# Kernel optimization log

Hardware: AMD Instinct MI355X
Metric: run time of the kernel (lower is better)

Reference implementation:

```python
import jax, jax.numpy as jnp
import numpy as np

B, L, D = 1, 512, 1280


def setup_inputs() -> dict:
    key = jax.random.key(0)
    k1, k2, k3 = jax.random.split(key, 3)
    prev_result = jax.random.normal(k1, (B, L, D), dtype=jnp.float32)
    # nn.Linear(2*D, 2): store weight as [2D, 2] so forward is x @ W + b
    W = jax.random.normal(k2, (2 * D, 2), dtype=jnp.float32) * (1.0 / np.sqrt(2 * D))
    b = jax.random.normal(k3, (2,), dtype=jnp.float32) * 0.01
    return {"prev_result": prev_result, "W": W, "b": b}


def reference(prev_result, W, b):
    # Dropout is identity at inference. The torch code builds
    # pairwise = cat(x_i * x_j, x_i - x_j) of shape [B,L,L,2D] then applies
    # Linear(2D, 2). We fuse: split W into the prod half Wp and diff half Wd.
    Wp, Wd = W[:D], W[D:]                                   # each [D, 2]
    # (x_i * x_j) @ Wp  -- bilinear contraction, no [B,L,L,2D] intermediate
    prod_term = jnp.einsum('bid,bjd,dk->bijk', prev_result, prev_result, Wp)
    # (x_i - x_j) @ Wd = (x @ Wd)_i - (x @ Wd)_j
    d_proj = prev_result @ Wd                                # [B, L, 2]
    diff_term = d_proj[:, :, None, :] - d_proj[:, None, :, :]
    prediction = prod_term + diff_term + b                   # [B, L, L, 2]
    prediction = (prediction + prediction.transpose(0, 2, 1, 3)) / 2
    return prediction[:, 1:-1, 1:-1]                         # [B, L-2, L-2, 2]
```

## Files before the change

kernel.cpp:

```cpp
#include <hip/hip_runtime.h>

#define D_DIM 1280
#define ODIM  510
#define NSTEP (D_DIM / 32)

typedef __attribute__((ext_vector_type(8))) short bf16x8;
typedef __attribute__((ext_vector_type(4))) float f32x4;

__device__ __forceinline__ unsigned pkbf(float a, float b) {
  unsigned ua = __float_as_uint(a), ub = __float_as_uint(b);
  return ((ua + 0x8000u) >> 16) | ((ub + 0x8000u) & 0xffff0000u);
}

__global__ __launch_bounds__(256, 1) void pcmd_prep(
    const float* __restrict__ X,
    const float* __restrict__ W,
    unsigned short* __restrict__ Xbf,
    unsigned short* __restrict__ A0,
    unsigned short* __restrict__ A1)
{
  int t = (int)blockIdx.x * 256 + (int)threadIdx.x;
  int r = t / 160;
  int c = t - r * 160;
  const float* px = X + (size_t)r * D_DIM + c * 8;
  float4 x0 = *(const float4*)px;
  float4 x1 = *(const float4*)(px + 4);
  const float* pw = W + (size_t)c * 16;
  float4 w0 = *(const float4*)(pw +  0);
  float4 w1 = *(const float4*)(pw +  4);
  float4 w2 = *(const float4*)(pw +  8);
  float4 w3 = *(const float4*)(pw + 12);
  size_t o = (size_t)r * D_DIM + c * 8;
  uint4 vx, v0, v1;
  vx.x = pkbf(x0.x, x0.y);            vx.y = pkbf(x0.z, x0.w);
  vx.z = pkbf(x1.x, x1.y);            vx.w = pkbf(x1.z, x1.w);
  v0.x = pkbf(x0.x*w0.x, x0.y*w0.z);  v0.y = pkbf(x0.z*w1.x, x0.w*w1.z);
  v0.z = pkbf(x1.x*w2.x, x1.y*w2.z);  v0.w = pkbf(x1.z*w3.x, x1.w*w3.z);
  v1.x = pkbf(x0.x*w0.y, x0.y*w0.w);  v1.y = pkbf(x0.z*w1.y, x0.w*w1.w);
  v1.z = pkbf(x1.x*w2.y, x1.y*w2.w);  v1.w = pkbf(x1.z*w3.y, x1.w*w3.w);
  *(uint4*)(Xbf + o) = vx;
  *(uint4*)(A0  + o) = v0;
  *(uint4*)(A1  + o) = v1;
}

__global__ __launch_bounds__(256, 1) void pcmd_gemm(
    const unsigned short* __restrict__ Xbf,
    const unsigned short* __restrict__ A0,
    const unsigned short* __restrict__ A1,
    const float* __restrict__ b,
    float* __restrict__ out)
{
  const int tid  = threadIdx.x;
  const int lane = tid & 63;
  const int wv   = tid >> 6;
  const int wi   = wv >> 1;
  const int wj   = wv & 1;
  const int m    = lane & 15;
  const int quad = lane >> 4;

  const int i_base = 1 + (int)blockIdx.y * 32 + wi * 16;
  const int j_base = 1 + (int)blockIdx.x * 32 + wj * 16;
  int gi = i_base + m; if (gi > 511) gi = 511;
  int gj = j_base + m; if (gj > 511) gj = 511;

  const unsigned short* pa0 = A0  + (size_t)gi * D_DIM + quad * 8;
  const unsigned short* pa1 = A1  + (size_t)gi * D_DIM + quad * 8;
  const unsigned short* pb  = Xbf + (size_t)gj * D_DIM + quad * 8;

  bf16x8 ra0[4], ra1[4], rb[4];
  #pragma unroll
  for (int s = 0; s < 4; ++s) {
    ra0[s] = *(const bf16x8*)(pa0 + s * 32);
    ra1[s] = *(const bf16x8*)(pa1 + s * 32);
    rb[s]  = *(const bf16x8*)(pb  + s * 32);
  }

  f32x4 acc0 = {0.f, 0.f, 0.f, 0.f};
  f32x4 acc1 = {0.f, 0.f, 0.f, 0.f};

  #pragma unroll 4
  for (int s = 0; s < NSTEP; ++s) {
    int cur = s & 3;
    bf16x8 a0 = ra0[cur], a1 = ra1[cur], bb = rb[cur];
    if (s + 4 < NSTEP) {
      ra0[cur] = *(const bf16x8*)(pa0 + (s + 4) * 32);
      ra1[cur] = *(const bf16x8*)(pa1 + (s + 4) * 32);
      rb[cur]  = *(const bf16x8*)(pb  + (s + 4) * 32);
    }
    acc0 = __builtin_amdgcn_mfma_f32_16x16x32_bf16(a0, bb, acc0, 0, 0, 0);
    acc1 = __builtin_amdgcn_mfma_f32_16x16x32_bf16(a1, bb, acc1, 0, 0, 0);
  }

  const float b0 = b[0], b1 = b[1];
  const int j = j_base + m;
  #pragma unroll
  for (int r = 0; r < 4; ++r) {
    int i = i_base + quad * 4 + r;
    if (i <= ODIM && j <= ODIM) {
      float2 v;
      v.x = acc0[r] + b0;
      v.y = acc1[r] + b1;
      *(float2*)(out + ((size_t)(i - 1) * ODIM + (j - 1)) * 2) = v;
    }
  }
}

extern "C" void kernel_launch(void* const* d_in, const int* in_sizes, int n_in,
                              void* d_out, int out_size, void* d_ws, size_t ws_size,
                              hipStream_t stream) {
  const float* X = (const float*)d_in[0];
  const float* W = (const float*)d_in[1];
  const float* b = (const float*)d_in[2];
  float* out = (float*)d_out;
  (void)in_sizes; (void)n_in; (void)out_size; (void)ws_size;

  const size_t PLANE = (size_t)512 * D_DIM;
  unsigned short* Xbf = (unsigned short*)d_ws;
  unsigned short* A0  = Xbf + PLANE;
  unsigned short* A1  = A0 + PLANE;

  hipLaunchKernelGGL(pcmd_prep, dim3(320), dim3(256), 0, stream, X, W, Xbf, A0, A1);
  hipLaunchKernelGGL(pcmd_gemm, dim3(16, 16), dim3(256), 0, stream, Xbf, A0, A1, b, out);
}
```

Before: 75.70 us.

## Split K across waves with LDS reduction and use smaller output tiles

The GEMM kernel now gives each block a 16x16 output tile and splits the 1280-long reduction across its four waves, summing the partial accumulators through shared memory. Launching four times as many blocks with higher occupancy shortens each wave's serial MFMA chain and fills more CUs. In exchange, smaller tiles double operand reloads from cache, and a barrier plus LDS reduction is added. The prep kernel also switches to nontemporal stores for its bf16 outputs.

```diff
diff --git a/kernel.cpp b/kernel.cpp
--- a/kernel.cpp
+++ b/kernel.cpp
@@ -2,10 +2,10 @@
 
 #define D_DIM 1280
 #define ODIM  510
-#define NSTEP (D_DIM / 32)
 
-typedef __attribute__((ext_vector_type(8))) short bf16x8;
-typedef __attribute__((ext_vector_type(4))) float f32x4;
+typedef short bf16x8 __attribute__((ext_vector_type(8)));
+typedef float f32x4  __attribute__((ext_vector_type(4)));
+typedef unsigned uint4n __attribute__((ext_vector_type(4)));
 
 __device__ __forceinline__ unsigned pkbf(float a, float b) {
   unsigned ua = __float_as_uint(a), ub = __float_as_uint(b);
@@ -31,41 +31,42 @@
   float4 w2 = *(const float4*)(pw +  8);
   float4 w3 = *(const float4*)(pw + 12);
   size_t o = (size_t)r * D_DIM + c * 8;
-  uint4 vx, v0, v1;
+  uint4n vx, v0, v1;
   vx.x = pkbf(x0.x, x0.y);            vx.y = pkbf(x0.z, x0.w);
   vx.z = pkbf(x1.x, x1.y);            vx.w = pkbf(x1.z, x1.w);
   v0.x = pkbf(x0.x*w0.x, x0.y*w0.z);  v0.y = pkbf(x0.z*w1.x, x0.w*w1.z);
   v0.z = pkbf(x1.x*w2.x, x1.y*w2.z);  v0.w = pkbf(x1.z*w3.x, x1.w*w3.z);
   v1.x = pkbf(x0.x*w0.y, x0.y*w0.w);  v1.y = pkbf(x0.z*w1.y, x0.w*w1.w);
   v1.z = pkbf(x1.x*w2.y, x1.y*w2.w);  v1.w = pkbf(x1.z*w3.y, x1.w*w3.w);
-  *(uint4*)(Xbf + o) = vx;
-  *(uint4*)(A0  + o) = v0;
-  *(uint4*)(A1  + o) = v1;
+  __builtin_nontemporal_store(vx, (uint4n*)(Xbf + o));
+  __builtin_nontemporal_store(v0, (uint4n*)(A0  + o));
+  __builtin_nontemporal_store(v1, (uint4n*)(A1  + o));
 }
 
-__global__ __launch_bounds__(256, 1) void pcmd_gemm(
+__global__ __launch_bounds__(256, 4) void pcmd_gemm(
     const unsigned short* __restrict__ Xbf,
     const unsigned short* __restrict__ A0,
     const unsigned short* __restrict__ A1,
     const float* __restrict__ b,
     float* __restrict__ out)
 {
+  __shared__ float sR[4][2][16][16];
+
   const int tid  = threadIdx.x;
   const int lane = tid & 63;
   const int wv   = tid >> 6;
-  const int wi   = wv >> 1;
-  const int wj   = wv & 1;
   const int m    = lane & 15;
   const int quad = lane >> 4;
 
-  const int i_base = 1 + (int)blockIdx.y * 32 + wi * 16;
-  const int j_base = 1 + (int)blockIdx.x * 32 + wj * 16;
+  const int i_base = 1 + (int)blockIdx.y * 16;
+  const int j_base = 1 + (int)blockIdx.x * 16;
   int gi = i_base + m; if (gi > 511) gi = 511;
   int gj = j_base + m; if (gj > 511) gj = 511;
 
-  const unsigned short* pa0 = A0  + (size_t)gi * D_DIM + quad * 8;
-  const unsigned short* pa1 = A1  + (size_t)gi * D_DIM + quad * 8;
-  const unsigned short* pb  = Xbf + (size_t)gj * D_DIM + quad * 8;
+  const int k0 = wv * 320;
+  const unsigned short* pa0 = A0  + (size_t)gi * D_DIM + k0 + quad * 8;
+  const unsigned short* pa1 = A1  + (size_t)gi * D_DIM + k0 + quad * 8;
+  const unsigned short* pb  = Xbf + (size_t)gj * D_DIM + k0 + quad * 8;
 
   bf16x8 ra0[4], ra1[4], rb[4];
   #pragma unroll
@@ -78,11 +79,11 @@
   f32x4 acc0 = {0.f, 0.f, 0.f, 0.f};
   f32x4 acc1 = {0.f, 0.f, 0.f, 0.f};
 
-  #pragma unroll 4
-  for (int s = 0; s < NSTEP; ++s) {
+  #pragma unroll
+  for (int s = 0; s < 10; ++s) {
     int cur = s & 3;
     bf16x8 a0 = ra0[cur], a1 = ra1[cur], bb = rb[cur];
-    if (s + 4 < NSTEP) {
+    if (s + 4 < 10) {
       ra0[cur] = *(const bf16x8*)(pa0 + (s + 4) * 32);
       ra1[cur] = *(const bf16x8*)(pa1 + (s + 4) * 32);
       rb[cur]  = *(const bf16x8*)(pb  + (s + 4) * 32);
@@ -91,17 +92,20 @@
     acc1 = __builtin_amdgcn_mfma_f32_16x16x32_bf16(a1, bb, acc1, 0, 0, 0);
   }
 
-  const float b0 = b[0], b1 = b[1];
-  const int j = j_base + m;
   #pragma unroll
   for (int r = 0; r < 4; ++r) {
-    int i = i_base + quad * 4 + r;
-    if (i <= ODIM && j <= ODIM) {
-      float2 v;
-      v.x = acc0[r] + b0;
-      v.y = acc1[r] + b1;
-      *(float2*)(out + ((size_t)(i - 1) * ODIM + (j - 1)) * 2) = v;
-    }
+    sR[wv][0][quad * 4 + r][m] = acc0[r];
+    sR[wv][1][quad * 4 + r][m] = acc1[r];
+  }
+  __syncthreads();
+
+  const int il = tid >> 4, jl = tid & 15;
+  const int i = i_base + il, j = j_base + jl;
+  if (i <= ODIM && j <= ODIM) {
+    float2 v;
+    v.x = sR[0][0][il][jl] + sR[1][0][il][jl] + sR[2][0][il][jl] + sR[3][0][il][jl] + b[0];
+    v.y = sR[0][1][il][jl] + sR[1][1][il][jl] + sR[2][1][il][jl] + sR[3][1][il][jl] + b[1];
+    *(float2*)(out + ((size_t)(i - 1) * ODIM + (j - 1)) * 2) = v;
   }
 }
 
@@ -120,5 +124,5 @@
   unsigned short* A1  = A0 + PLANE;
 
   hipLaunchKernelGGL(pcmd_prep, dim3(320), dim3(256), 0, stream, X, W, Xbf, A0, A1);
-  hipLaunchKernelGGL(pcmd_gemm, dim3(16, 16), dim3(256), 0, stream, Xbf, A0, A1, b, out);
+  hipLaunchKernelGGL(pcmd_gemm, dim3(32, 32), dim3(256), 0, stream, Xbf, A0, A1, b, out);
 }
```

Result: slower. 77.45 us (+2.3%).
